# Performance work log

Hardware: AMD Instinct MI355X
Metric: run time of the kernel (lower is better)

## Reference

```python
import jax, jax.numpy as jnp
import numpy as np

DECAY_MIN = 2.0
DECAY_MAX = 2.0


def setup_inputs() -> dict:
    key = jax.random.key(0)
    k1, k2, k3 = jax.random.split(key, 3)
    x = jax.random.normal(k1, (16, 256, 4096), dtype=jnp.float32)
    kernels = jax.random.normal(k2, (6, 4, 256, 32), dtype=jnp.float32)
    D = jax.random.normal(k3, (4, 256), dtype=jnp.float32)
    return {"x": x, "kernels": kernels, "D": D}


def _build_kernel(kernels):
    # kernels: (num_scales, heads, h, kernel_size)
    num_scales, heads, h, ks = kernels.shape
    multiplier = jnp.linspace(DECAY_MIN, DECAY_MAX, h).reshape(1, -1, 1)  # (1, h, 1)
    parts = []
    for i in range(num_scales):
        rep = 2 ** max(0, i - 1)
        ker = jnp.repeat(kernels[i], rep, axis=-1)  # nearest-neighbor upsample
        parts.append(ker * multiplier ** (num_scales - i - 1))
    k = jnp.concatenate(parts, axis=-1)  # (heads, h, kernel_length)
    # kernel_norm is computed on first forward and detached
    norm = jax.lax.stop_gradient(
        jnp.linalg.norm(k, axis=-1, keepdims=True))
    return k / norm


def reference(x, kernels, D):
    # x: (b, h, L); kernels: (S, heads, h, ks); D: (heads, h)
    b, h, L = x.shape
    heads = kernels.shape[1]
    k = _build_kernel(kernels)                 # (heads, h, KL)
    kernel_length = k.shape[-1]
    n = 2 * L                                  # 'constant' padding mode -> factor 2
    k_f = jnp.fft.rfft(k, n=n)                 # (heads, h, n//2+1)
    u_f = jnp.fft.rfft(x, n=n)                 # (b, h, n//2+1)
    y_f = jnp.einsum('bhl,chl->bchl', u_f, k_f)
    y = jnp.fft.irfft(y_f, n=n)                # (b, heads, h, n)
    s = kernel_length // 2
    y = y[..., s:s + L]                        # (b, heads, h, L)
    # rearrange 'b c h l -> b (h c) l'
    y = jnp.transpose(y, (0, 2, 1, 3)).reshape(b, h * heads, L)
    skip = jnp.einsum('bhl,ch->bchl', x, D)    # (b, heads, h, L)
    skip = jnp.transpose(skip, (0, 2, 1, 3)).reshape(b, h * heads, L)
    return y + skip
```

## Files before the change

kernel.cpp:

```cpp
#include <hip/hip_runtime.h>

#define HEADS 4
#define NH    256
#define LEN   4096
#define NB    16
#define TT    1024
#define NSUB  4

typedef float     f32x4 __attribute__((ext_vector_type(4)));
typedef _Float16  f16x2 __attribute__((ext_vector_type(2)));
typedef _Float16  f16x8 __attribute__((ext_vector_type(8)));
typedef unsigned  u32x2 __attribute__((ext_vector_type(2)));
typedef unsigned  u32x4 __attribute__((ext_vector_type(4)));

__device__ __forceinline__ unsigned packh(float a, float b) {
    union { _Float16 h[2]; unsigned u; } z;
    z.h[0] = (_Float16)a; z.h[1] = (_Float16)b;
    return z.u;
}
__device__ __forceinline__ unsigned short h16u(float a) {
    union { _Float16 h; unsigned short u; } z;
    z.h = (_Float16)a; return z.u;
}
__device__ __forceinline__ float lo16(unsigned u) {
    return (float)__builtin_bit_cast(f16x2, u)[0];
}
__device__ __forceinline__ float hi16(unsigned u) {
    return (float)__builtin_bit_cast(f16x2, u)[1];
}

__global__ __launch_bounds__(64) void build_wgt_kernel(
    const float* __restrict__ kernels, unsigned short* __restrict__ wtab)
{
    const int h    = blockIdx.x;
    const int lane = threadIdx.x;

    float ssum[4] = {0.f, 0.f, 0.f, 0.f};
    #pragma unroll
    for (int q = 0; q < 3; ++q) {
        const int tap = lane + q * 64;
        const int i = tap >> 5;
        const int j = tap & 31;
        const float scale = (float)(1 << (5 - i));
        const float repf  = (float)(i == 0 ? 1 : (1 << (i - 1)));
        #pragma unroll
        for (int c = 0; c < 4; ++c) {
            const float kv = kernels[(((i * HEADS) + c) * NH + h) * 32 + j];
            const float v  = kv * scale;
            ssum[c] += v * v * repf;
        }
    }
    #pragma unroll
    for (int off = 32; off > 0; off >>= 1) {
        #pragma unroll
        for (int c = 0; c < 4; ++c) ssum[c] += __shfl_xor(ssum[c], off);
    }
    float inv[4];
    #pragma unroll
    for (int c = 0; c < 4; ++c) inv[c] = 1.0f / sqrtf(ssum[c]);

    for (int it = 0; it < 40; ++it) {
        const int idx = it * 64 + lane;
        const int c   = idx / 640;
        const int rem = idx - c * 640;
        const int u   = rem >> 7;
        const int y   = rem & 127;
        const int j   = 95 - y;
        const int J   = (u == 0) ? 64 : 32;
        float val = 0.f;
        if (j >= 0 && j < J) {
            int s, tp;
            if (u == 0) { s = (j < 32) ? 0 : 1; tp = j & 31; }
            else        { s = u + 1;            tp = j;      }
            val = kernels[((s * HEADS + c) * NH + h) * 32 + tp]
                  * (float)(1 << (5 - s)) * inv[c];
        }
        wtab[((h * 4 + c) * 5 + u) * 128 + y] = h16u(val);
    }
}

#define AFB   0
#define GBASE 22528
#define G1B   (GBASE + 0)
#define G2B   (GBASE + 4160)
#define G4B   (GBASE + 8256)
#define G8B   (GBASE + 12352)
#define G16B  (GBASE + 16448)
#define DRB   43072
#define SMBYTES 48192

#define SWZ(BASE, OFF, SH, MSK) \
    ((char*)SM + (BASE) + ((OFF) ^ ((((OFF) >> (SH)) & (MSK)) << 4)))

#define AFRD(F) (*(const f16x8*)((char*)SM + AFB + (F) * 1024 + lane * 16))

#define MFMA16(acc, a, bb) \
    (acc) = __builtin_amdgcn_mfma_f32_16x16x32_f16((a), (bb), (acc), 0, 0, 0)

__global__ __launch_bounds__(256, 3) void conv_kernel(
    const float*           __restrict__ x,
    const unsigned short*  __restrict__ wtab,
    const float*           __restrict__ Dp,
    float*                 __restrict__ out)
{
    __shared__ __align__(16) unsigned char SM[SMBYTES];
    unsigned* DR32 = (unsigned*)(SM + DRB);

    const int cpair = blockIdx.x;
    const int h     = blockIdx.y;
    const int b     = blockIdx.z;
    const int tid   = threadIdx.x;
    const int w     = tid >> 6;
    const int lane  = tid & 63;
    const int dd    = lane & 15;
    const int qq    = lane >> 4;

    const float* xrow = x + ((size_t)(b * NH + h)) * LEN;

    if (w == 0) {
        #pragma unroll
        for (int cc = 0; cc < 2; ++cc) {
            const int c = cpair * 2 + cc;
            const unsigned short* wpc = wtab + (size_t)((h * 4 + c) * 5) * 128;
            #pragma unroll
            for (int u = 0; u < 5; ++u) {
                const int J   = (u == 0) ? 64 : 32;
                const int nM  = (u == 0) ? 3 : 2;
                const int bse = (u == 0) ? 0 : (2 * u + 1);
                const unsigned short* wp = wpc + u * 128;
                #pragma unroll
                for (int m = 0; m < 3; ++m) {
                    if (m < nM) {
                        const int y0 = 95 - dd - J + 32 * m + 8 * qq;
                        u32x4 dw;
                        #pragma unroll
                        for (int d = 0; d < 4; ++d)
                            dw[d] = (unsigned)wp[y0 + 2 * d]
                                  | ((unsigned)wp[y0 + 2 * d + 1] << 16);
                        const int f = cc * 11 + bse + m;
                        *(u32x4*)((char*)SM + AFB + f * 1024 + lane * 16) = dw;
                    }
                }
            }
        }
    }
    if (tid < 4)
        *(u32x4*)SWZ(G1B - GBASE + GBASE, 4096 + 16 * tid, 7, 1) = (u32x4){0,0,0,0};

    const float dC0 = Dp[(cpair * 2 + 0) * NH + h];
    const float dC1 = Dp[(cpair * 2 + 1) * NH + h];

    const int kap = 16 * w + dd;
    const int E0B = 32 * kap + 1920 + 16 * qq;
    const int E1B = 2048 * (kap & 1)  + 32 * (kap >> 1) + 896 + 16 * qq;
    const int E2B = 1024 * (kap & 3)  + 32 * (kap >> 2) + 384 + 16 * qq;
    const int E3B = 512  * (kap & 7)  + 32 * (kap >> 3) + 128 + 16 * qq;
    const int E4B = 256  * (kap & 15) + 32 * (kap >> 4)       + 16 * qq;

    for (int st = 0; st < NSUB; ++st) {
        const int t0s = st * TT;
        __syncthreads();

        {
            const int bg = t0s - 544 + 8 * tid;
            float v[40];
            #pragma unroll
            for (int blk = 0; blk < 10; ++blk) {
                const int g = bg + 4 * blk;
                f32x4 t;
                if (g >= 0 && g + 3 < LEN) {
                    t = *(const f32x4*)(xrow + g);
                } else {
                    #pragma unroll
                    for (int e = 0; e < 4; ++e) {
                        const int gg = g + e;
                        t[e] = (gg >= 0 && gg < LEN) ? xrow[gg] : 0.f;
                    }
                }
                v[4 * blk] = t.x; v[4 * blk + 1] = t.y;
                v[4 * blk + 2] = t.z; v[4 * blk + 3] = t.w;
            }
            {
                u32x4 px;
                px[0] = packh(v[32], v[33]); px[1] = packh(v[34], v[35]);
                px[2] = packh(v[36], v[37]); px[3] = packh(v[38], v[39]);
                *(u32x4*)SWZ(G1B, 16 * tid, 7, 1) = px;
            }
            #pragma unroll
            for (int j = 39; j >= 2; --j) v[j] += v[j - 1];
            #pragma unroll
            for (int ph = 0; ph < 2; ++ph) {
                u32x2 pw;
                pw.x = packh(v[32 + ph], v[34 + ph]);
                pw.y = packh(v[36 + ph], v[38 + ph]);
                *(u32x2*)SWZ(G2B, 2048 * ph + 8 * tid, 7, 1) = pw;
            }
            #pragma unroll
            for (int j = 39; j >= 4; --j) v[j] += v[j - 2];
            #pragma unroll
            for (int ph = 0; ph < 4; ++ph)
                *(unsigned*)SWZ(G4B, 1024 * ph + 4 * tid, 10, 1) =
                    packh(v[32 + ph], v[36 + ph]);
            #pragma unroll
            for (int j = 39; j >= 8; --j) v[j] += v[j - 4];
            #pragma unroll
            for (int e = 0; e < 8; ++e)
                *(unsigned short*)SWZ(G8B, 512 * e + 2 * tid, 9, 7) =
                    h16u(v[32 + e]);
            #pragma unroll
            for (int j = 39; j >= 16; --j) v[j] += v[j - 8];
            #pragma unroll
            for (int e = 0; e < 8; ++e) {
                const int E = 8 * (tid & 1) + e;
                *(unsigned short*)SWZ(G16B, 256 * E + 2 * (tid >> 1), 8, 7) =
                    h16u(v[32 + e]);
            }
        }
        __syncthreads();

        f32x4 DA[2][5];
        #pragma unroll
        for (int cc = 0; cc < 2; ++cc)
            #pragma unroll
            for (int u = 0; u < 5; ++u) DA[cc][u] = (f32x4){0.f, 0.f, 0.f, 0.f};

        {
            const f16x8 b0 = *(const f16x8*)SWZ(G1B, E0B,       7, 1);
            const f16x8 b1 = *(const f16x8*)SWZ(G1B, E0B + 64,  7, 1);
            const f16x8 b2 = *(const f16x8*)SWZ(G1B, E0B + 128, 7, 1);
            MFMA16(DA[0][0], AFRD(0),  b0); MFMA16(DA[0][0], AFRD(1),  b1);
            MFMA16(DA[0][0], AFRD(2),  b2);
            MFMA16(DA[1][0], AFRD(11), b0); MFMA16(DA[1][0], AFRD(12), b1);
            MFMA16(DA[1][0], AFRD(13), b2);
        }
        {
            const f16x8 b0 = *(const f16x8*)SWZ(G2B, E1B,      7, 1);
            const f16x8 b1 = *(const f16x8*)SWZ(G2B, E1B + 64, 7, 1);
            MFMA16(DA[0][1], AFRD(3),  b0); MFMA16(DA[0][1], AFRD(4),  b1);
            MFMA16(DA[1][1], AFRD(14), b0); MFMA16(DA[1][1], AFRD(15), b1);
        }
        {
            const f16x8 b0 = *(const f16x8*)SWZ(G4B, E2B,      10, 1);
            const f16x8 b1 = *(const f16x8*)SWZ(G4B, E2B + 64, 10, 1);
            MFMA16(DA[0][2], AFRD(5),  b0); MFMA16(DA[0][2], AFRD(6),  b1);
            MFMA16(DA[1][2], AFRD(16), b0); MFMA16(DA[1][2], AFRD(17), b1);
        }
        {
            const f16x8 b0 = *(const f16x8*)SWZ(G8B, E3B,      9, 7);
            const f16x8 b1 = *(const f16x8*)SWZ(G8B, E3B + 64, 9, 7);
            MFMA16(DA[0][3], AFRD(7),  b0); MFMA16(DA[0][3], AFRD(8),  b1);
            MFMA16(DA[1][3], AFRD(18), b0); MFMA16(DA[1][3], AFRD(19), b1);
        }
        {
            const f16x8 b0 = *(const f16x8*)SWZ(G16B, E4B,      8, 7);
            const f16x8 b1 = *(const f16x8*)SWZ(G16B, E4B + 64, 8, 7);
            MFMA16(DA[0][4], AFRD(9),  b0); MFMA16(DA[0][4], AFRD(10), b1);
            MFMA16(DA[1][4], AFRD(20), b0); MFMA16(DA[1][4], AFRD(21), b1);
        }

        f32x4 a0 = (f32x4){0.f,0.f,0.f,0.f};
        f32x4 a1 = (f32x4){0.f,0.f,0.f,0.f};

#define DRWRITE(U) do {                                                   \
        const int row_ = w * 64 + lane;                                   \
        _Pragma("unroll")                                                 \
        for (int e = 0; e < 4; ++e)                                       \
            DR32[row_ * 5 + e] = packh(DA[0][U][e], DA[1][U][e]);         \
    } while (0)

        {
            DRWRITE(0);
            const int sL = (lane >> 2) + 16 * (lane & 3);
            const int rb = (w * 64 + sL) * 5;
            #pragma unroll
            for (int e = 0; e < 4; ++e) {
                const unsigned q = DR32[rb + e];
                a0[e] += lo16(q); a1[e] += hi16(q);
            }
        }
        {
            DRWRITE(1);
            const int da = (2 * lane) & 15;
            const int uu = lane >> 3;
            const int L  = 2 * uu + 16 * (da >> 2);
            const int bi = (w * 64 + L) * 5 + (da & 3);
            const unsigned qa = DR32[bi],     qb = DR32[bi + 1];
            const unsigned qc = DR32[bi + 5], qd = DR32[bi + 6];
            a0[0] += lo16(qa); a1[0] += hi16(qa);
            a0[2] += lo16(qb); a1[2] += hi16(qb);
            a0[1] += lo16(qc); a1[1] += hi16(qc);
            a0[3] += lo16(qd); a1[3] += hi16(qd);
        }
        {
            DRWRITE(2);
            const int de = lane & 15;
            const int uu = lane >> 4;
            const int L0 = 4 * uu + 16 * (de >> 2);
            const int rb = w * 64 + L0;
            #pragma unroll
            for (int e = 0; e < 4; ++e) {
                const unsigned q = DR32[(rb + e) * 5 + (de & 3)];
                a0[e] += lo16(q); a1[e] += hi16(q);
            }
        }
        {
            DRWRITE(3);
            const int de = (lane >> 1) & 15;
            const int uu = lane >> 5;
            const int L0 = 8 * uu + 4 * (lane & 1) + 16 * (de >> 2);
            const int rb = w * 64 + L0;
            #pragma unroll
            for (int e = 0; e < 4; ++e) {
                const unsigned q = DR32[(rb + e) * 5 + (de & 3)];
                a0[e] += lo16(q); a1[e] += hi16(q);
            }
        }
        {
            DRWRITE(4);
            const int de = (lane >> 2) & 15;
            const int L0 = 4 * (lane & 3) + 16 * (de >> 2);
            const int rb = w * 64 + L0;
            #pragma unroll
            for (int e = 0; e < 4; ++e) {
                const unsigned q = DR32[(rb + e) * 5 + (de & 3)];
                a0[e] += lo16(q); a1[e] += hi16(q);
            }
        }
#undef DRWRITE

        const int gt = t0s + 256 * w + 4 * lane;
        const f32x4 xv = *(const f32x4*)(xrow + gt);
        const size_t ob = ((size_t)(b * NH + h) * 4 + cpair * 2) * LEN + gt;
        *(f32x4*)(out + ob)       = a0 + xv * dC0;
        *(f32x4*)(out + ob + LEN) = a1 + xv * dC1;
    }
}

extern "C" void kernel_launch(void* const* d_in, const int* in_sizes, int n_in,
                              void* d_out, int out_size, void* d_ws, size_t ws_size,
                              hipStream_t stream)
{
    const float* x       = (const float*)d_in[0];
    const float* kernels = (const float*)d_in[1];
    const float* D       = (const float*)d_in[2];
    float*       out     = (float*)d_out;
    unsigned short* wtab = (unsigned short*)d_ws;

    build_wgt_kernel<<<256, 64, 0, stream>>>(kernels, wtab);
    conv_kernel<<<dim3(2, NH, NB), 256, 0, stream>>>(x, wtab, D, out);
}
```

Baseline: 164.9 us.

## Process all four heads per block to reuse the prefix-sum input staging

```diff
diff --git a/kernel.cpp b/kernel.cpp
--- a/kernel.cpp
+++ b/kernel.cpp
@@ -80,14 +80,14 @@
 }
 
 #define AFB   0
-#define GBASE 22528
+#define GBASE 45056
 #define G1B   (GBASE + 0)
 #define G2B   (GBASE + 4160)
 #define G4B   (GBASE + 8256)
 #define G8B   (GBASE + 12352)
 #define G16B  (GBASE + 16448)
-#define DRB   43072
-#define SMBYTES 48192
+#define DRB   65600
+#define SMBYTES 70720
 
 #define SWZ(BASE, OFF, SH, MSK) \
     ((char*)SM + (BASE) + ((OFF) ^ ((((OFF) >> (SH)) & (MSK)) << 4)))
@@ -97,18 +97,17 @@
 #define MFMA16(acc, a, bb) \
     (acc) = __builtin_amdgcn_mfma_f32_16x16x32_f16((a), (bb), (acc), 0, 0, 0)
 
-__global__ __launch_bounds__(256, 3) void conv_kernel(
+__global__ __launch_bounds__(256, 2) void conv_kernel(
     const float*           __restrict__ x,
     const unsigned short*  __restrict__ wtab,
     const float*           __restrict__ Dp,
     float*                 __restrict__ out)
 {
-    __shared__ __align__(16) unsigned char SM[SMBYTES];
+    extern __shared__ __align__(16) unsigned char SM[];
     unsigned* DR32 = (unsigned*)(SM + DRB);
 
-    const int cpair = blockIdx.x;
-    const int h     = blockIdx.y;
-    const int b     = blockIdx.z;
+    const int h     = blockIdx.x;
+    const int b     = blockIdx.y;
     const int tid   = threadIdx.x;
     const int w     = tid >> 6;
     const int lane  = tid & 63;
@@ -117,38 +116,37 @@
 
     const float* xrow = x + ((size_t)(b * NH + h)) * LEN;
 
-    if (w == 0) {
-        #pragma unroll
-        for (int cc = 0; cc < 2; ++cc) {
-            const int c = cpair * 2 + cc;
-            const unsigned short* wpc = wtab + (size_t)((h * 4 + c) * 5) * 128;
-            #pragma unroll
-            for (int u = 0; u < 5; ++u) {
-                const int J   = (u == 0) ? 64 : 32;
-                const int nM  = (u == 0) ? 3 : 2;
-                const int bse = (u == 0) ? 0 : (2 * u + 1);
-                const unsigned short* wp = wpc + u * 128;
-                #pragma unroll
-                for (int m = 0; m < 3; ++m) {
-                    if (m < nM) {
-                        const int y0 = 95 - dd - J + 32 * m + 8 * qq;
-                        u32x4 dw;
-                        #pragma unroll
-                        for (int d = 0; d < 4; ++d)
-                            dw[d] = (unsigned)wp[y0 + 2 * d]
-                                  | ((unsigned)wp[y0 + 2 * d + 1] << 16);
-                        const int f = cc * 11 + bse + m;
-                        *(u32x4*)((char*)SM + AFB + f * 1024 + lane * 16) = dw;
-                    }
+    {
+        const int c = w;
+        const unsigned short* wpc = wtab + (size_t)((h * 4 + c) * 5) * 128;
+        #pragma unroll
+        for (int u = 0; u < 5; ++u) {
+            const int J   = (u == 0) ? 64 : 32;
+            const int nM  = (u == 0) ? 3 : 2;
+            const int bse = (u == 0) ? 0 : (2 * u + 1);
+            const unsigned short* wp = wpc + u * 128;
+            #pragma unroll
+            for (int m = 0; m < 3; ++m) {
+                if (m < nM) {
+                    const int y0 = 95 - dd - J + 32 * m + 8 * qq;
+                    u32x4 dw;
+                    #pragma unroll
+                    for (int d = 0; d < 4; ++d)
+                        dw[d] = (unsigned)wp[y0 + 2 * d]
+                              | ((unsigned)wp[y0 + 2 * d + 1] << 16);
+                    const int f = c * 11 + bse + m;
+                    *(u32x4*)((char*)SM + AFB + f * 1024 + lane * 16) = dw;
                 }
             }
         }
     }
     if (tid < 4)
-        *(u32x4*)SWZ(G1B - GBASE + GBASE, 4096 + 16 * tid, 7, 1) = (u32x4){0,0,0,0};
-
-    const float dC0 = Dp[(cpair * 2 + 0) * NH + h];
-    const float dC1 = Dp[(cpair * 2 + 1) * NH + h];
+        *(u32x4*)SWZ(G1B, 4096 + 16 * tid, 7, 1) = (u32x4){0, 0, 0, 0};
+
+    const float dC0 = Dp[0 * NH + h];
+    const float dC1 = Dp[1 * NH + h];
+    const float dC2 = Dp[2 * NH + h];
+    const float dC3 = Dp[3 * NH + h];
 
     const int kap = 16 * w + dd;
     const int E0B = 32 * kap + 1920 + 16 * qq;
@@ -218,121 +216,141 @@
         }
         __syncthreads();
 
-        f32x4 DA[2][5];
-        #pragma unroll
-        for (int cc = 0; cc < 2; ++cc)
-            #pragma unroll
-            for (int u = 0; u < 5; ++u) DA[cc][u] = (f32x4){0.f, 0.f, 0.f, 0.f};
+        f32x4 DA[4][5];
+        #pragma unroll
+        for (int c = 0; c < 4; ++c)
+            #pragma unroll
+            for (int u = 0; u < 5; ++u) DA[c][u] = (f32x4){0.f, 0.f, 0.f, 0.f};
 
         {
             const f16x8 b0 = *(const f16x8*)SWZ(G1B, E0B,       7, 1);
             const f16x8 b1 = *(const f16x8*)SWZ(G1B, E0B + 64,  7, 1);
             const f16x8 b2 = *(const f16x8*)SWZ(G1B, E0B + 128, 7, 1);
-            MFMA16(DA[0][0], AFRD(0),  b0); MFMA16(DA[0][0], AFRD(1),  b1);
-            MFMA16(DA[0][0], AFRD(2),  b2);
-            MFMA16(DA[1][0], AFRD(11), b0); MFMA16(DA[1][0], AFRD(12), b1);
-            MFMA16(DA[1][0], AFRD(13), b2);
+            #pragma unroll
+            for (int c = 0; c < 4; ++c) {
+                MFMA16(DA[c][0], AFRD(c * 11 + 0), b0);
+                MFMA16(DA[c][0], AFRD(c * 11 + 1), b1);
+                MFMA16(DA[c][0], AFRD(c * 11 + 2), b2);
+            }
         }
         {
             const f16x8 b0 = *(const f16x8*)SWZ(G2B, E1B,      7, 1);
             const f16x8 b1 = *(const f16x8*)SWZ(G2B, E1B + 64, 7, 1);
-            MFMA16(DA[0][1], AFRD(3),  b0); MFMA16(DA[0][1], AFRD(4),  b1);
-            MFMA16(DA[1][1], AFRD(14), b0); MFMA16(DA[1][1], AFRD(15), b1);
+            #pragma unroll
+            for (int c = 0; c < 4; ++c) {
+                MFMA16(DA[c][1], AFRD(c * 11 + 3), b0);
+                MFMA16(DA[c][1], AFRD(c * 11 + 4), b1);
+            }
         }
         {
             const f16x8 b0 = *(const f16x8*)SWZ(G4B, E2B,      10, 1);
             const f16x8 b1 = *(const f16x8*)SWZ(G4B, E2B + 64, 10, 1);
-            MFMA16(DA[0][2], AFRD(5),  b0); MFMA16(DA[0][2], AFRD(6),  b1);
-            MFMA16(DA[1][2], AFRD(16), b0); MFMA16(DA[1][2], AFRD(17), b1);
+            #pragma unroll
+            for (int c = 0; c < 4; ++c) {
+                MFMA16(DA[c][2], AFRD(c * 11 + 5), b0);
+                MFMA16(DA[c][2], AFRD(c * 11 + 6), b1);
+            }
         }
         {
             const f16x8 b0 = *(const f16x8*)SWZ(G8B, E3B,      9, 7);
             const f16x8 b1 = *(const f16x8*)SWZ(G8B, E3B + 64, 9, 7);
-            MFMA16(DA[0][3], AFRD(7),  b0); MFMA16(DA[0][3], AFRD(8),  b1);
-            MFMA16(DA[1][3], AFRD(18), b0); MFMA16(DA[1][3], AFRD(19), b1);
+            #pragma unroll
+            for (int c = 0; c < 4; ++c) {
+                MFMA16(DA[c][3], AFRD(c * 11 + 7), b0);
+                MFMA16(DA[c][3], AFRD(c * 11 + 8), b1);
+            }
         }
         {
             const f16x8 b0 = *(const f16x8*)SWZ(G16B, E4B,      8, 7);
             const f16x8 b1 = *(const f16x8*)SWZ(G16B, E4B + 64, 8, 7);
-            MFMA16(DA[0][4], AFRD(9),  b0); MFMA16(DA[0][4], AFRD(10), b1);
-            MFMA16(DA[1][4], AFRD(20), b0); MFMA16(DA[1][4], AFRD(21), b1);
-        }
-
-        f32x4 a0 = (f32x4){0.f,0.f,0.f,0.f};
-        f32x4 a1 = (f32x4){0.f,0.f,0.f,0.f};
-
-#define DRWRITE(U) do {                                                   \
-        const int row_ = w * 64 + lane;                                   \
-        _Pragma("unroll")                                                 \
-        for (int e = 0; e < 4; ++e)                                       \
-            DR32[row_ * 5 + e] = packh(DA[0][U][e], DA[1][U][e]);         \
-    } while (0)
-
-        {
-            DRWRITE(0);
-            const int sL = (lane >> 2) + 16 * (lane & 3);
-            const int rb = (w * 64 + sL) * 5;
-            #pragma unroll
-            for (int e = 0; e < 4; ++e) {
-                const unsigned q = DR32[rb + e];
-                a0[e] += lo16(q); a1[e] += hi16(q);
-            }
-        }
-        {
-            DRWRITE(1);
-            const int da = (2 * lane) & 15;
-            const int uu = lane >> 3;
-            const int L  = 2 * uu + 16 * (da >> 2);
-            const int bi = (w * 64 + L) * 5 + (da & 3);
-            const unsigned qa = DR32[bi],     qb = DR32[bi + 1];
-            const unsigned qc = DR32[bi + 5], qd = DR32[bi + 6];
-            a0[0] += lo16(qa); a1[0] += hi16(qa);
-            a0[2] += lo16(qb); a1[2] += hi16(qb);
-            a0[1] += lo16(qc); a1[1] += hi16(qc);
-            a0[3] += lo16(qd); a1[3] += hi16(qd);
-        }
-        {
-            DRWRITE(2);
-            const int de = lane & 15;
-            const int uu = lane >> 4;
-            const int L0 = 4 * uu + 16 * (de >> 2);
-            const int rb = w * 64 + L0;
-            #pragma unroll
-            for (int e = 0; e < 4; ++e) {
-                const unsigned q = DR32[(rb + e) * 5 + (de & 3)];
-                a0[e] += lo16(q); a1[e] += hi16(q);
-            }
-        }
-        {
-            DRWRITE(3);
-            const int de = (lane >> 1) & 15;
-            const int uu = lane >> 5;
-            const int L0 = 8 * uu + 4 * (lane & 1) + 16 * (de >> 2);
-            const int rb = w * 64 + L0;
-            #pragma unroll
-            for (int e = 0; e < 4; ++e) {
-                const unsigned q = DR32[(rb + e) * 5 + (de & 3)];
-                a0[e] += lo16(q); a1[e] += hi16(q);
-            }
-        }
-        {
-            DRWRITE(4);
-            const int de = (lane >> 2) & 15;
-            const int L0 = 4 * (lane & 3) + 16 * (de >> 2);
-            const int rb = w * 64 + L0;
-            #pragma unroll
-            for (int e = 0; e < 4; ++e) {
-                const unsigned q = DR32[(rb + e) * 5 + (de & 3)];
-                a0[e] += lo16(q); a1[e] += hi16(q);
-            }
-        }
-#undef DRWRITE
+            #pragma unroll
+            for (int c = 0; c < 4; ++c) {
+                MFMA16(DA[c][4], AFRD(c * 11 + 9),  b0);
+                MFMA16(DA[c][4], AFRD(c * 11 + 10), b1);
+            }
+        }
 
         const int gt = t0s + 256 * w + 4 * lane;
         const f32x4 xv = *(const f32x4*)(xrow + gt);
-        const size_t ob = ((size_t)(b * NH + h) * 4 + cpair * 2) * LEN + gt;
-        *(f32x4*)(out + ob)       = a0 + xv * dC0;
-        *(f32x4*)(out + ob + LEN) = a1 + xv * dC1;
+        const size_t ob = ((size_t)(b * NH + h) * 4) * LEN + gt;
+
+        #pragma unroll
+        for (int p = 0; p < 2; ++p) {
+            f32x4 a0 = (f32x4){0.f, 0.f, 0.f, 0.f};
+            f32x4 a1 = (f32x4){0.f, 0.f, 0.f, 0.f};
+
+#define DRWRITE(U) do {                                                    \
+        const int row_ = w * 64 + lane;                                    \
+        _Pragma("unroll")                                                  \
+        for (int e = 0; e < 4; ++e)                                        \
+            DR32[row_ * 5 + e] = packh(DA[2 * p][U][e], DA[2 * p + 1][U][e]); \
+    } while (0)
+
+            {
+                DRWRITE(0);
+                const int sL = (lane >> 2) + 16 * (lane & 3);
+                const int rb = (w * 64 + sL) * 5;
+                #pragma unroll
+                for (int e = 0; e < 4; ++e) {
+                    const unsigned q = DR32[rb + e];
+                    a0[e] += lo16(q); a1[e] += hi16(q);
+                }
+            }
+            {
+                DRWRITE(1);
+                const int da = (2 * lane) & 15;
+                const int uu = lane >> 3;
+                const int L  = 2 * uu + 16 * (da >> 2);
+                const int bi = (w * 64 + L) * 5 + (da & 3);
+                const unsigned qa = DR32[bi],     qb = DR32[bi + 1];
+                const unsigned qc = DR32[bi + 5], qd = DR32[bi + 6];
+                a0[0] += lo16(qa); a1[0] += hi16(qa);
+                a0[2] += lo16(qb); a1[2] += hi16(qb);
+                a0[1] += lo16(qc); a1[1] += hi16(qc);
+                a0[3] += lo16(qd); a1[3] += hi16(qd);
+            }
+            {
+                DRWRITE(2);
+                const int de = lane & 15;
+                const int uu = lane >> 4;
+                const int L0 = 4 * uu + 16 * (de >> 2);
+                const int rb = w * 64 + L0;
+                #pragma unroll
+                for (int e = 0; e < 4; ++e) {
+                    const unsigned q = DR32[(rb + e) * 5 + (de & 3)];
+                    a0[e] += lo16(q); a1[e] += hi16(q);
+                }
+            }
+            {
+                DRWRITE(3);
+                const int de = (lane >> 1) & 15;
+                const int uu = lane >> 5;
+                const int L0 = 8 * uu + 4 * (lane & 1) + 16 * (de >> 2);
+                const int rb = w * 64 + L0;
+                #pragma unroll
+                for (int e = 0; e < 4; ++e) {
+                    const unsigned q = DR32[(rb + e) * 5 + (de & 3)];
+                    a0[e] += lo16(q); a1[e] += hi16(q);
+                }
+            }
+            {
+                DRWRITE(4);
+                const int de = (lane >> 2) & 15;
+                const int L0 = 4 * (lane & 3) + 16 * (de >> 2);
+                const int rb = w * 64 + L0;
+                #pragma unroll
+                for (int e = 0; e < 4; ++e) {
+                    const unsigned q = DR32[(rb + e) * 5 + (de & 3)];
+                    a0[e] += lo16(q); a1[e] += hi16(q);
+                }
+            }
+#undef DRWRITE
+
+            const float dA = (p == 0) ? dC0 : dC2;
+            const float dB = (p == 0) ? dC1 : dC3;
+            *(f32x4*)(out + ob + (size_t)(2 * p)     * LEN) = a0 + xv * dA;
+            *(f32x4*)(out + ob + (size_t)(2 * p + 1) * LEN) = a1 + xv * dB;
+        }
     }
 }
 
@@ -346,6 +364,10 @@
     float*       out     = (float*)d_out;
     unsigned short* wtab = (unsigned short*)d_ws;
 
+    (void)hipFuncSetAttribute((const void*)conv_kernel,
+                              hipFuncAttributeMaxDynamicSharedMemorySize,
+                              SMBYTES);
+
     build_wgt_kernel<<<256, 64, 0, stream>>>(kernels, wtab);
-    conv_kernel<<<dim3(2, NH, NB), 256, 0, stream>>>(x, wtab, D, out);
-}
+    conv_kernel<<<dim3(NH, NB), 256, SMBYTES, stream>>>(x, wtab, D, out);
+}
```

Result: slower. 176.5 us (+7.0%).

## Compact weight fragments and alias reduction buffer to fit four blocks per CU

Applied to the files above, without the earlier changes.

```diff
diff --git a/kernel.cpp b/kernel.cpp
--- a/kernel.cpp
+++ b/kernel.cpp
@@ -8,6 +8,7 @@
 #define NSUB  4
 
 typedef float     f32x4 __attribute__((ext_vector_type(4)));
+typedef float     f32x2 __attribute__((ext_vector_type(2)));
 typedef _Float16  f16x2 __attribute__((ext_vector_type(2)));
 typedef _Float16  f16x8 __attribute__((ext_vector_type(8)));
 typedef unsigned  u32x2 __attribute__((ext_vector_type(2)));
@@ -80,31 +81,35 @@
 }
 
 #define AFB   0
-#define GBASE 22528
+#define HFB   12288
+#define ZPB   17408
+#define GBASE 17920
 #define G1B   (GBASE + 0)
 #define G2B   (GBASE + 4160)
 #define G4B   (GBASE + 8256)
 #define G8B   (GBASE + 12352)
 #define G16B  (GBASE + 16448)
-#define DRB   43072
-#define SMBYTES 48192
+#define SMBYTES 38464
 
 #define SWZ(BASE, OFF, SH, MSK) \
     ((char*)SM + (BASE) + ((OFF) ^ ((((OFF) >> (SH)) & (MSK)) << 4)))
 
-#define AFRD(F) (*(const f16x8*)((char*)SM + AFB + (F) * 1024 + lane * 16))
+#define AFF(CC, FI) \
+    (*(const f16x8*)((char*)SM + AFB + ((CC) * 6 + (FI)) * 1024 + lane * 16))
+#define AFH(CC, HI) \
+    (*(const f16x8*)((char*)SM + hbase + (hmask & (((CC) * 5 + (HI)) * 512))))
 
 #define MFMA16(acc, a, bb) \
     (acc) = __builtin_amdgcn_mfma_f32_16x16x32_f16((a), (bb), (acc), 0, 0, 0)
 
-__global__ __launch_bounds__(256, 3) void conv_kernel(
+__global__ __launch_bounds__(256, 4) void conv_kernel(
     const float*           __restrict__ x,
     const unsigned short*  __restrict__ wtab,
     const float*           __restrict__ Dp,
     float*                 __restrict__ out)
 {
     __shared__ __align__(16) unsigned char SM[SMBYTES];
-    unsigned* DR32 = (unsigned*)(SM + DRB);
+    unsigned* DR32 = (unsigned*)(SM + GBASE);
 
     const int cpair = blockIdx.x;
     const int h     = blockIdx.y;
@@ -124,9 +129,8 @@
             const unsigned short* wpc = wtab + (size_t)((h * 4 + c) * 5) * 128;
             #pragma unroll
             for (int u = 0; u < 5; ++u) {
-                const int J   = (u == 0) ? 64 : 32;
-                const int nM  = (u == 0) ? 3 : 2;
-                const int bse = (u == 0) ? 0 : (2 * u + 1);
+                const int J  = (u == 0) ? 64 : 32;
+                const int nM = (u == 0) ? 3 : 2;
                 const unsigned short* wp = wpc + u * 128;
                 #pragma unroll
                 for (int m = 0; m < 3; ++m) {
@@ -137,18 +141,27 @@
                         for (int d = 0; d < 4; ++d)
                             dw[d] = (unsigned)wp[y0 + 2 * d]
                                   | ((unsigned)wp[y0 + 2 * d + 1] << 16);
-                        const int f = cc * 11 + bse + m;
-                        *(u32x4*)((char*)SM + AFB + f * 1024 + lane * 16) = dw;
+                        if (m == nM - 1) {
+                            if (lane < 32)
+                                *(u32x4*)((char*)SM + HFB
+                                    + (cc * 5 + u) * 512 + lane * 16) = dw;
+                        } else {
+                            const int fi = (u == 0) ? m : u + 1;
+                            *(u32x4*)((char*)SM + AFB
+                                + (cc * 6 + fi) * 1024 + lane * 16) = dw;
+                        }
                     }
                 }
             }
         }
     }
-    if (tid < 4)
-        *(u32x4*)SWZ(G1B - GBASE + GBASE, 4096 + 16 * tid, 7, 1) = (u32x4){0,0,0,0};
+    if (tid < 32) *(u32x4*)((char*)SM + ZPB + tid * 16) = (u32x4){0, 0, 0, 0};
 
     const float dC0 = Dp[(cpair * 2 + 0) * NH + h];
     const float dC1 = Dp[(cpair * 2 + 1) * NH + h];
+
+    const int hbase = (lane < 32) ? (HFB + lane * 16) : (ZPB + (lane - 32) * 16);
+    const int hmask = (lane < 32) ? ~0 : 0;
 
     const int kap = 16 * w + dd;
     const int E0B = 32 * kap + 1920 + 16 * qq;
@@ -186,6 +199,9 @@
                 px[2] = packh(v[36], v[37]); px[3] = packh(v[38], v[39]);
                 *(u32x4*)SWZ(G1B, 16 * tid, 7, 1) = px;
             }
+            if (tid < 4)
+                *(u32x4*)SWZ(G1B, 4096 + 16 * tid, 7, 1) = (u32x4){0, 0, 0, 0};
+
             #pragma unroll
             for (int j = 39; j >= 2; --j) v[j] += v[j - 1];
             #pragma unroll
@@ -228,38 +244,53 @@
             const f16x8 b0 = *(const f16x8*)SWZ(G1B, E0B,       7, 1);
             const f16x8 b1 = *(const f16x8*)SWZ(G1B, E0B + 64,  7, 1);
             const f16x8 b2 = *(const f16x8*)SWZ(G1B, E0B + 128, 7, 1);
-            MFMA16(DA[0][0], AFRD(0),  b0); MFMA16(DA[0][0], AFRD(1),  b1);
-            MFMA16(DA[0][0], AFRD(2),  b2);
-            MFMA16(DA[1][0], AFRD(11), b0); MFMA16(DA[1][0], AFRD(12), b1);
-            MFMA16(DA[1][0], AFRD(13), b2);
+            #pragma unroll
+            for (int cc = 0; cc < 2; ++cc) {
+                MFMA16(DA[cc][0], AFF(cc, 0), b0);
+                MFMA16(DA[cc][0], AFF(cc, 1), b1);
+                MFMA16(DA[cc][0], AFH(cc, 0), b2);
+            }
         }
         {
             const f16x8 b0 = *(const f16x8*)SWZ(G2B, E1B,      7, 1);
             const f16x8 b1 = *(const f16x8*)SWZ(G2B, E1B + 64, 7, 1);
-            MFMA16(DA[0][1], AFRD(3),  b0); MFMA16(DA[0][1], AFRD(4),  b1);
-            MFMA16(DA[1][1], AFRD(14), b0); MFMA16(DA[1][1], AFRD(15), b1);
+            #pragma unroll
+            for (int cc = 0; cc < 2; ++cc) {
+                MFMA16(DA[cc][1], AFF(cc, 2), b0);
+                MFMA16(DA[cc][1], AFH(cc, 1), b1);
+            }
         }
         {
             const f16x8 b0 = *(const f16x8*)SWZ(G4B, E2B,      10, 1);
             const f16x8 b1 = *(const f16x8*)SWZ(G4B, E2B + 64, 10, 1);
-            MFMA16(DA[0][2], AFRD(5),  b0); MFMA16(DA[0][2], AFRD(6),  b1);
-            MFMA16(DA[1][2], AFRD(16), b0); MFMA16(DA[1][2], AFRD(17), b1);
+            #pragma unroll
+            for (int cc = 0; cc < 2; ++cc) {
+                MFMA16(DA[cc][2], AFF(cc, 3), b0);
+                MFMA16(DA[cc][2], AFH(cc, 2), b1);
+            }
         }
         {
             const f16x8 b0 = *(const f16x8*)SWZ(G8B, E3B,      9, 7);
             const f16x8 b1 = *(const f16x8*)SWZ(G8B, E3B + 64, 9, 7);
-            MFMA16(DA[0][3], AFRD(7),  b0); MFMA16(DA[0][3], AFRD(8),  b1);
-            MFMA16(DA[1][3], AFRD(18), b0); MFMA16(DA[1][3], AFRD(19), b1);
+            #pragma unroll
+            for (int cc = 0; cc < 2; ++cc) {
+                MFMA16(DA[cc][3], AFF(cc, 4), b0);
+                MFMA16(DA[cc][3], AFH(cc, 3), b1);
+            }
         }
         {
             const f16x8 b0 = *(const f16x8*)SWZ(G16B, E4B,      8, 7);
             const f16x8 b1 = *(const f16x8*)SWZ(G16B, E4B + 64, 8, 7);
-            MFMA16(DA[0][4], AFRD(9),  b0); MFMA16(DA[0][4], AFRD(10), b1);
-            MFMA16(DA[1][4], AFRD(20), b0); MFMA16(DA[1][4], AFRD(21), b1);
-        }
-
-        f32x4 a0 = (f32x4){0.f,0.f,0.f,0.f};
-        f32x4 a1 = (f32x4){0.f,0.f,0.f,0.f};
+            #pragma unroll
+            for (int cc = 0; cc < 2; ++cc) {
+                MFMA16(DA[cc][4], AFF(cc, 5), b0);
+                MFMA16(DA[cc][4], AFH(cc, 4), b1);
+            }
+        }
+        __syncthreads();
+
+        f32x4 a0 = (f32x4){0.f, 0.f, 0.f, 0.f};
+        f32x4 a1 = (f32x4){0.f, 0.f, 0.f, 0.f};
 
 #define DRWRITE(U) do {                                                   \
         const int row_ = w * 64 + lane;                                   \
```

Result: no change. 165.4 us (+0.3%).
